# Optimization experiments

Measured on AMD Instinct MI355X. Metric: run time of the kernel, lower is better.

## Reference

```python
import jax, jax.numpy as jnp
import numpy as np

HIDDEN = 768
HEADS = 12
HEAD_DIM = HIDDEN // HEADS


def setup_inputs() -> dict:
    key = jax.random.key(0)
    ks = jax.random.split(key, 6)
    B, N = 32, 577  # N = 1 CLS + 576 patches
    x = jax.random.normal(ks[0], (B, N, HIDDEN), dtype=jnp.float32)
    seg_bias = jax.random.uniform(ks[1], (B, N - 1), dtype=jnp.float32)
    w_qkv = jax.random.normal(ks[2], (HIDDEN, 3 * HIDDEN), dtype=jnp.float32) * 0.02
    b_qkv = jnp.zeros((3 * HIDDEN,), dtype=jnp.float32)
    w_proj = jax.random.normal(ks[3], (HIDDEN, HIDDEN), dtype=jnp.float32) * 0.02
    b_proj = jnp.zeros((HIDDEN,), dtype=jnp.float32)
    seg_scale = jnp.ones((), dtype=jnp.float32)
    return {"x": x, "seg_bias": seg_bias, "w_qkv": w_qkv, "b_qkv": b_qkv,
            "w_proj": w_proj, "b_proj": b_proj, "seg_scale": seg_scale}


def reference(x, seg_bias, w_qkv, b_qkv, w_proj, b_proj, seg_scale):
    B, N, _ = x.shape
    scale = HEAD_DIM ** -0.5
    qkv = x @ w_qkv + b_qkv                       # (B, N, 3*H*D)
    qkv = qkv.reshape(B, N, 3, HEADS, HEAD_DIM)
    q = qkv[:, :, 0].transpose(0, 2, 1, 3)        # (B, H, N, D)
    k = qkv[:, :, 1].transpose(0, 2, 1, 3)
    v = qkv[:, :, 2].transpose(0, 2, 1, 3)
    attn = jnp.einsum('bhqd,bhkd->bhqk', q, k) * scale  # (B, H, N, N)
    # additive seg bias on CLS-query row, patch keys only (cols 1:)
    bias = (seg_bias * seg_scale)[:, None, None, :]     # (B,1,1,N-1)
    attn = attn.at[:, :, 0:1, 1:].add(bias)
    attn = jax.nn.softmax(attn, axis=-1)
    out = jnp.einsum('bhqk,bhkd->bhqd', attn, v)        # (B, H, N, D)
    out = out.transpose(0, 2, 1, 3).reshape(B, N, HIDDEN)
    return out @ w_proj + b_proj
```

## Files before the change

### kernel.cpp

```cpp
#include <hip/hip_runtime.h>


typedef unsigned short bf16_t;
typedef __attribute__((ext_vector_type(8))) short short8;
typedef __attribute__((ext_vector_type(4))) short short4v;
typedef __attribute__((ext_vector_type(4))) float f32x4;

#define B_    32
#define N_    577
#define BN_   18464
#define HID_  768
#define NH_   12
#define HD_   64
#define QKVC_ 2304
#define NPAD_ 640
#define PB_LD 68

__device__ __forceinline__ bf16_t f2bf(float f) {
  union { float f; unsigned u; } x; x.f = f;
  unsigned r = x.u + 0x7fffu + ((x.u >> 16) & 1u);
  return (bf16_t)(r >> 16);
}

__device__ __forceinline__ unsigned cvt_pk_bf16(float a, float b) {
  unsigned r;
  asm("v_cvt_pk_bf16_f32 %0, %1, %2" : "=v"(r) : "v"(a), "v"(b));
  return r;
}

__global__ __launch_bounds__(256) void cast_kernel(const float* __restrict__ in,
                                                   bf16_t* __restrict__ out, int n4) {
  int i = blockIdx.x * 256 + threadIdx.x;
  if (i >= n4) return;
  float4 v = ((const float4*)in)[i];
  ushort4 o;
  o.x = f2bf(v.x); o.y = f2bf(v.y); o.z = f2bf(v.z); o.w = f2bf(v.w);
  ((ushort4*)out)[i] = o;
}

__global__ __launch_bounds__(256) void transpose_cast_kernel(const float* __restrict__ in,
                                                             bf16_t* __restrict__ out,
                                                             int R, int C) {
  __shared__ float tile[32][33];
  int c0 = blockIdx.x * 32, r0 = blockIdx.y * 32;
  int tx = threadIdx.x, ty = threadIdx.y;
  #pragma unroll
  for (int i = ty; i < 32; i += 8)
    tile[i][tx] = in[(size_t)(r0 + i) * C + c0 + tx];
  __syncthreads();
  #pragma unroll
  for (int i = ty; i < 32; i += 8)
    out[(size_t)(c0 + i) * R + r0 + tx] = f2bf(tile[tx][i]);
}

template <int OUT_BF16>
__global__ __launch_bounds__(256, 3) void gemm_bf16_kernel(
    const bf16_t* __restrict__ A,
    const bf16_t* __restrict__ Bt,
    const float* __restrict__ bias,
    void* __restrict__ Cout,
    int M, int Nc) {
  __shared__ bf16_t As[128 * 64];
  __shared__ bf16_t Bs[128 * 64];

  const int tid  = threadIdx.x;
  const int lane = tid & 63, w = tid >> 6;
  const int quad = lane >> 4, l16 = lane & 15;

  const int Mb = (M + 127) >> 7;
  const int Nb = Nc >> 7;
  const int np_full = Mb >> 3;
  const int rem = Mb - np_full * 8;
  int bid = blockIdx.x;
  int m_blk, n_blk;
  int body = np_full * 8 * Nb;
  if (bid < body) {
    int p = bid / (8 * Nb), local = bid % (8 * Nb);
    m_blk = p * 8 + (local & 7);
    n_blk = local >> 3;
  } else {
    int t = bid - body;
    m_blk = np_full * 8 + t % rem;
    n_blk = t / rem;
  }
  const int m0 = m_blk * 128, n0 = n_blk * 128;
  const int wm = (w >> 1) * 64, wn = (w & 1) * 64;

  f32x4 acc[4][4];
  #pragma unroll
  for (int i = 0; i < 4; ++i)
    #pragma unroll
    for (int j = 0; j < 4; ++j)
      acc[i][j] = (f32x4){0.f, 0.f, 0.f, 0.f};

  for (int kt = 0; kt < 768; kt += 64) {
    __syncthreads();
    #pragma unroll
    for (int it = 0; it < 4; ++it) {
      int gi = it * 256 + tid;
      int row = gi >> 3, chp = gi & 7;
      int ch = chp ^ (row & 7);
      int gm = m0 + row; if (gm >= M) gm = M - 1;
      __builtin_amdgcn_global_load_lds(
          (const __attribute__((address_space(1))) unsigned int*)(A + (size_t)gm * 768 + kt + ch * 8),
          (__attribute__((address_space(3))) unsigned int*)(As + gi * 8),
          16, 0, 0);
      int gn = n0 + row;
      __builtin_amdgcn_global_load_lds(
          (const __attribute__((address_space(1))) unsigned int*)(Bt + (size_t)gn * 768 + kt + ch * 8),
          (__attribute__((address_space(3))) unsigned int*)(Bs + gi * 8),
          16, 0, 0);
    }
    __syncthreads();

    #pragma unroll
    for (int ks = 0; ks < 2; ++ks) {
      short8 af[4], bfr[4];
      #pragma unroll
      for (int i = 0; i < 4; ++i) {
        int row = wm + i * 16 + l16;
        int c = ks * 4 + quad;
        af[i] = *(const short8*)(As + row * 64 + (c ^ (row & 7)) * 8);
      }
      #pragma unroll
      for (int j = 0; j < 4; ++j) {
        int row = wn + j * 16 + l16;
        int c = ks * 4 + quad;
        bfr[j] = *(const short8*)(Bs + row * 64 + (c ^ (row & 7)) * 8);
      }
      #pragma unroll
      for (int i = 0; i < 4; ++i)
        #pragma unroll
        for (int j = 0; j < 4; ++j)
          acc[i][j] = __builtin_amdgcn_mfma_f32_16x16x32_bf16(af[i], bfr[j], acc[i][j], 0, 0, 0);
    }
  }

  #pragma unroll
  for (int i = 0; i < 4; ++i) {
    int mrow_base = m0 + wm + i * 16 + quad * 4;
    #pragma unroll
    for (int j = 0; j < 4; ++j) {
      int col = n0 + wn + j * 16 + l16;
      float bs = bias[col];
      #pragma unroll
      for (int r = 0; r < 4; ++r) {
        int row = mrow_base + r;
        if (row < M) {
          float v = acc[i][j][r] + bs;
          if (OUT_BF16)
            ((bf16_t*)Cout)[(size_t)row * Nc + col] = f2bf(v);
          else
            ((float*)Cout)[(size_t)row * Nc + col] = v;
        }
      }
    }
  }
}

__global__ __launch_bounds__(256) void vt_kernel(const bf16_t* __restrict__ qkv,
                                                 bf16_t* __restrict__ vT) {
  const int t = blockIdx.x, h = blockIdx.y, b = blockIdx.z;
  const int tid = threadIdx.x;
  __shared__ bf16_t Ls[64 * 65];
  const int kv0 = t * 64;
  const bf16_t* Vp = qkv + (size_t)b * N_ * QKVC_ + 2 * HID_ + h * HD_;

  #pragma unroll
  for (int it = 0; it < 2; ++it) {
    int idx = it * 256 + tid;
    int row = idx >> 3, ch = idx & 7;
    int krow = kv0 + row; if (krow > N_ - 1) krow = N_ - 1;
    short8 v8 = *(const short8*)(Vp + (size_t)krow * QKVC_ + ch * 8);
    #pragma unroll
    for (int j = 0; j < 8; ++j)
      Ls[(ch * 8 + j) * 65 + row] = (bf16_t)v8[j];
  }
  __syncthreads();
  bf16_t* outp = vT + ((size_t)(b * NH_ + h) * HD_) * NPAD_;
  #pragma unroll
  for (int it = 0; it < 2; ++it) {
    int idx = it * 256 + tid;
    int d = idx >> 3, kc = idx & 7;
    short8 o8;
    #pragma unroll
    for (int j = 0; j < 8; ++j) {
      int p = kc * 8 + j;
      int ky = ((p & 3) << 4) | (p >> 2);
      o8[j] = (short)Ls[d * 65 + ky];
    }
    *(short8*)(outp + (size_t)d * NPAD_ + kv0 + kc * 8) = o8;
  }
}

template <int MI>
__device__ __forceinline__ void attn_body(
    int b, int h, int qbase,
    const bf16_t* __restrict__ qkv, const bf16_t* __restrict__ vT,
    const float* __restrict__ seg_bias, const float* __restrict__ seg_scale,
    bf16_t* __restrict__ out,
    bf16_t* Ks0, bf16_t* Ks1, bf16_t* Vt0, bf16_t* Vt1, bf16_t* PbAll) {
  const int tid = threadIdx.x;
  const int w = tid >> 6, lane = tid & 63;
  const int quad = lane >> 4, l16 = lane & 15;
  const int xsw = l16 & 7;

  const bf16_t* Qbase = qkv + (size_t)b * N_ * QKVC_ + h * HD_;
  const bf16_t* Kbase = Qbase + HID_;
  const bf16_t* Vtb   = vT + ((size_t)(b * NH_ + h) * HD_) * NPAD_;

  const float ssl = seg_scale[0] * 1.44269504f;

  {
    int row = tid >> 3;
    int ch = (tid & 7) ^ (row & 7);
    __builtin_amdgcn_global_load_lds(
        (const __attribute__((address_space(1))) unsigned int*)(Kbase + (size_t)row * QKVC_ + ch * 8),
        (__attribute__((address_space(3))) unsigned int*)(Ks0 + tid * 8), 16, 0, 0);
    __builtin_amdgcn_global_load_lds(
        (const __attribute__((address_space(1))) unsigned int*)(Vtb + (size_t)row * NPAD_ + ch * 8),
        (__attribute__((address_space(3))) unsigned int*)(Vt0 + tid * 8), 16, 0, 0);
  }

  const int q0 = qbase + w * (MI * 16);
  short8 qf[MI][2];
  #pragma unroll
  for (int mi = 0; mi < MI; ++mi) {
    int qr = q0 + mi * 16 + l16;
    if (qr > N_ - 1) qr = N_ - 1;
    qf[mi][0] = *(const short8*)(Qbase + (size_t)qr * QKVC_ + quad * 8);
    qf[mi][1] = *(const short8*)(Qbase + (size_t)qr * QKVC_ + 32 + quad * 8);
  }
  const float qsc = 0.125f * 1.44269504f;
  #pragma unroll
  for (int mi = 0; mi < MI; ++mi)
    #pragma unroll
    for (int c = 0; c < 2; ++c)
      #pragma unroll
      for (int j = 0; j < 8; ++j) {
        unsigned u = ((unsigned)(unsigned short)qf[mi][c][j]) << 16;
        union { unsigned u; float f; } x; x.u = u;
        qf[mi][c][j] = (short)f2bf(x.f * qsc);
      }

  const f32x4 z4 = {0.f, 0.f, 0.f, 0.f};
  f32x4 o[MI][4];
  f32x4 ls[MI];
  #pragma unroll
  for (int mi = 0; mi < MI; ++mi) {
    ls[mi] = z4;
    #pragma unroll
    for (int j = 0; j < 4; ++j) o[mi][j] = z4;
  }

  short8 ones;
  #pragma unroll
  for (int j = 0; j < 8; ++j) ones[j] = (short)0x3F80;

  const bool bias_wave = (qbase == 0 && w == 0);
  bf16_t* pw = PbAll + w * 16 * PB_LD;

  for (int t = 0; t < 9; ++t) {
    const int cur = t & 1;

    __builtin_amdgcn_s_barrier();
    __builtin_amdgcn_sched_barrier(0);

    {
      const int kv1 = (t + 1) * 64;
      bf16_t* ksn = cur ? Ks0 : Ks1;
      bf16_t* vtn = cur ? Vt0 : Vt1;
      int row = tid >> 3;
      int ch = (tid & 7) ^ (row & 7);
      int krow = kv1 + row; if (krow > N_ - 1) krow = N_ - 1;
      __builtin_amdgcn_global_load_lds(
          (const __attribute__((address_space(1))) unsigned int*)(Kbase + (size_t)krow * QKVC_ + ch * 8),
          (__attribute__((address_space(3))) unsigned int*)(ksn + tid * 8), 16, 0, 0);
      __builtin_amdgcn_global_load_lds(
          (const __attribute__((address_space(1))) unsigned int*)(Vtb + (size_t)row * NPAD_ + kv1 + ch * 8),
          (__attribute__((address_space(3))) unsigned int*)(vtn + tid * 8), 16, 0, 0);
    }

    asm volatile("s_waitcnt vmcnt(2)" ::: "memory");
    __builtin_amdgcn_sched_barrier(0);
    __builtin_amdgcn_s_barrier();
    __builtin_amdgcn_sched_barrier(0);

    const bf16_t* ks = cur ? Ks1 : Ks0;
    const bf16_t* vt = cur ? Vt1 : Vt0;

    f32x4 s[MI][4];
    __builtin_amdgcn_s_setprio(1);
    #pragma unroll
    for (int sub = 0; sub < 4; ++sub) {
      short8 k0 = *(const short8*)(ks + (sub * 16 + l16) * 64 + (quad ^ xsw) * 8);
      short8 k1 = *(const short8*)(ks + (sub * 16 + l16) * 64 + ((4 + quad) ^ xsw) * 8);
      #pragma unroll
      for (int mi = 0; mi < MI; ++mi) {
        s[mi][sub] = __builtin_amdgcn_mfma_f32_16x16x32_bf16(qf[mi][0], k0, z4, 0, 0, 0);
        s[mi][sub] = __builtin_amdgcn_mfma_f32_16x16x32_bf16(qf[mi][1], k1, s[mi][sub], 0, 0, 0);
      }
    }
    __builtin_amdgcn_s_setprio(0);

    if (bias_wave && quad == 0) {
      const int kv0 = t * 64;
      #pragma unroll
      for (int sub = 0; sub < 4; ++sub) {
        int key = kv0 + sub * 16 + l16;
        if (key >= 1)
          s[0][sub][0] += seg_bias[b * (N_ - 1) + key - 1] * ssl;
      }
    }

    #pragma unroll
    for (int mi = 0; mi < MI; ++mi) {
      #pragma unroll
      for (int r = 0; r < 4; ++r) {
        float p0 = __builtin_amdgcn_exp2f(s[mi][0][r]);
        float p1 = __builtin_amdgcn_exp2f(s[mi][1][r]);
        float p2 = __builtin_amdgcn_exp2f(s[mi][2][r]);
        float p3 = __builtin_amdgcn_exp2f(s[mi][3][r]);
        uint2 pk;
        pk.x = cvt_pk_bf16(p0, p1);
        pk.y = cvt_pk_bf16(p2, p3);
        *(uint2*)(pw + (quad * 4 + r) * PB_LD + l16 * 4) = pk;
      }

      const bf16_t* pr = pw + l16 * PB_LD + quad * 8;
      union { short8 v; short4v hv[2]; } pa0, pa1;
      pa0.hv[0] = *(const short4v*)(pr);
      pa0.hv[1] = *(const short4v*)(pr + 4);
      pa1.hv[0] = *(const short4v*)(pr + 32);
      pa1.hv[1] = *(const short4v*)(pr + 36);
      __builtin_amdgcn_s_setprio(1);
      ls[mi] = __builtin_amdgcn_mfma_f32_16x16x32_bf16(pa0.v, ones, ls[mi], 0, 0, 0);
      ls[mi] = __builtin_amdgcn_mfma_f32_16x16x32_bf16(pa1.v, ones, ls[mi], 0, 0, 0);
      #pragma unroll
      for (int ds = 0; ds < 4; ++ds) {
        short8 vb0 = *(const short8*)(vt + (ds * 16 + l16) * 64 + (quad ^ xsw) * 8);
        short8 vb1 = *(const short8*)(vt + (ds * 16 + l16) * 64 + ((4 + quad) ^ xsw) * 8);
        o[mi][ds] = __builtin_amdgcn_mfma_f32_16x16x32_bf16(pa0.v, vb0, o[mi][ds], 0, 0, 0);
        o[mi][ds] = __builtin_amdgcn_mfma_f32_16x16x32_bf16(pa1.v, vb1, o[mi][ds], 0, 0, 0);
      }
      __builtin_amdgcn_s_setprio(0);
    }
  }

  {
    asm volatile("s_waitcnt vmcnt(0)" ::: "memory");
    __builtin_amdgcn_sched_barrier(0);
    __builtin_amdgcn_s_barrier();
    __builtin_amdgcn_sched_barrier(0);

    const bf16_t* ks = Ks1;
    const bf16_t* vt = Vt1;

    short8 k0 = *(const short8*)(ks + l16 * 64 + (quad ^ xsw) * 8);
    short8 k1 = *(const short8*)(ks + l16 * 64 + ((4 + quad) ^ xsw) * 8);
    f32x4 s9[MI];
    #pragma unroll
    for (int mi = 0; mi < MI; ++mi) {
      s9[mi] = __builtin_amdgcn_mfma_f32_16x16x32_bf16(qf[mi][0], k0, z4, 0, 0, 0);
      s9[mi] = __builtin_amdgcn_mfma_f32_16x16x32_bf16(qf[mi][1], k1, s9[mi], 0, 0, 0);
    }
    if (bias_wave && quad == 0 && l16 == 0)
      s9[0][0] += seg_bias[b * (N_ - 1) + (N_ - 2)] * ssl;

    #pragma unroll
    for (int mi = 0; mi < MI; ++mi) {
      #pragma unroll
      for (int r = 0; r < 4; ++r) {
        float p0 = (l16 == 0) ? __builtin_amdgcn_exp2f(s9[mi][r]) : 0.f;
        uint2 pk;
        pk.x = cvt_pk_bf16(p0, 0.f);
        pk.y = 0u;
        *(uint2*)(pw + (quad * 4 + r) * PB_LD + l16 * 4) = pk;
      }
      const bf16_t* pr = pw + l16 * PB_LD + quad * 8;
      union { short8 v; short4v hv[2]; } pa0;
      pa0.hv[0] = *(const short4v*)(pr);
      pa0.hv[1] = *(const short4v*)(pr + 4);
      ls[mi] = __builtin_amdgcn_mfma_f32_16x16x32_bf16(pa0.v, ones, ls[mi], 0, 0, 0);
      #pragma unroll
      for (int ds = 0; ds < 4; ++ds) {
        short8 vb0 = *(const short8*)(vt + (ds * 16 + l16) * 64 + (quad ^ xsw) * 8);
        o[mi][ds] = __builtin_amdgcn_mfma_f32_16x16x32_bf16(pa0.v, vb0, o[mi][ds], 0, 0, 0);
      }
    }
  }

  #pragma unroll
  for (int mi = 0; mi < MI; ++mi)
    #pragma unroll
    for (int r = 0; r < 4; ++r) {
      float inv = 1.0f / ls[mi][r];
      int row = q0 + mi * 16 + quad * 4 + r;
      if (row < N_) {
        size_t base = ((size_t)b * N_ + row) * HID_ + h * HD_;
        #pragma unroll
        for (int ds = 0; ds < 4; ++ds)
          out[base + ds * 16 + l16] = f2bf(o[mi][ds][r] * inv);
      }
    }
}

__global__ __launch_bounds__(512) void attn_kernel(
    const bf16_t* __restrict__ qkv,
    const bf16_t* __restrict__ vT,
    const float* __restrict__ seg_bias,
    const float* __restrict__ seg_scale,
    bf16_t* __restrict__ out) {
  __shared__ __align__(16) bf16_t Ks[2][64 * 64];
  __shared__ __align__(16) bf16_t Vt[2][64 * 64];
  __shared__ __align__(16) bf16_t Pb[8][16 * PB_LD];

  const int bid = blockIdx.x;
  if (bid < 768) {
    const int pair = bid % 384, qblk = bid / 384;
    attn_body<2>(pair / NH_, pair % NH_, qblk * 256,
                 qkv, vT, seg_bias, seg_scale, out,
                 &Ks[0][0], &Ks[1][0], &Vt[0][0], &Vt[1][0], &Pb[0][0]);
  } else {
    const int pair = bid - 768;
    attn_body<1>(pair / NH_, pair % NH_, 512,
                 qkv, vT, seg_bias, seg_scale, out,
                 &Ks[0][0], &Ks[1][0], &Vt[0][0], &Vt[1][0], &Pb[0][0]);
  }
}

extern "C" void kernel_launch(void* const* d_in, const int* in_sizes, int n_in,
                              void* d_out, int out_size, void* d_ws, size_t ws_size,
                              hipStream_t stream) {
  const float* x         = (const float*)d_in[0];
  const float* seg_bias  = (const float*)d_in[1];
  const float* w_qkv     = (const float*)d_in[2];
  const float* b_qkv     = (const float*)d_in[3];
  const float* w_proj    = (const float*)d_in[4];
  const float* b_proj    = (const float*)d_in[5];
  const float* seg_scale = (const float*)d_in[6];

  char* ws = (char*)d_ws;
  bf16_t* xb     = (bf16_t*)ws;
  bf16_t* wqkvT  = (bf16_t*)(ws + 28360704);
  bf16_t* wprojT = (bf16_t*)(ws + 31899648);
  bf16_t* qkvb   = (bf16_t*)(ws + 33079296);
  bf16_t* vT     = (bf16_t*)(ws + 118161408);
  bf16_t* attnb  = xb;

  cast_kernel<<<(BN_ * HID_ / 4) / 256, 256, 0, stream>>>(x, xb, BN_ * HID_ / 4);
  dim3 tb(32, 8);
  transpose_cast_kernel<<<dim3(QKVC_ / 32, HID_ / 32), tb, 0, stream>>>(w_qkv, wqkvT, HID_, QKVC_);
  transpose_cast_kernel<<<dim3(HID_ / 32, HID_ / 32), tb, 0, stream>>>(w_proj, wprojT, HID_, HID_);

  gemm_bf16_kernel<1><<<145 * (QKVC_ / 128), 256, 0, stream>>>(
      xb, wqkvT, b_qkv, (void*)qkvb, BN_, QKVC_);

  vt_kernel<<<dim3(10, NH_, B_), 256, 0, stream>>>(qkvb, vT);

  attn_kernel<<<1152, 512, 0, stream>>>(qkvb, vT, seg_bias, seg_scale, attnb);

  gemm_bf16_kernel<0><<<145 * (HID_ / 128), 256, 0, stream>>>(
      attnb, wprojT, b_proj, d_out, BN_, HID_);
}
```

Measured before the change: 302.3 us.

## Use 256x256 double-buffered GEMM tiles with async LDS prefetch

The bf16 GEMM kernel moves from 128x128 tiles with 256 threads to 256x256 tiles with 512 threads. Shared memory is double-buffered and the next K-slices are prefetched through global_load_lds, with explicit vmcnt waits and barriers in place of sync-load-sync. MFMA sections are wrapped in setprio. The aim is more data reuse per tile and overlap of global loads with compute, at the cost of 1 block per CU and coarse tiles that waste work on the M tail (18464 rows) and give fewer blocks for the 768-wide projection GEMM.

```diff
diff --git a/kernel.cpp b/kernel.cpp
--- a/kernel.cpp
+++ b/kernel.cpp
@@ -53,22 +53,43 @@
     out[(size_t)(c0 + i) * R + r0 + tx] = f2bf(tile[tx][i]);
 }
 
+__device__ __forceinline__ void stage256(const bf16_t* __restrict__ A,
+                                         const bf16_t* __restrict__ Bt,
+                                         int M, int m0, int n0, int kt,
+                                         bf16_t* as, bf16_t* bs, int tid) {
+  #pragma unroll
+  for (int it = 0; it < 4; ++it) {
+    int gi = it * 512 + tid;
+    int row = gi >> 3;
+    int ch = (gi & 7) ^ (row & 7);
+    int gm = m0 + row; if (gm >= M) gm = M - 1;
+    __builtin_amdgcn_global_load_lds(
+        (const __attribute__((address_space(1))) unsigned int*)(A + (size_t)gm * 768 + kt + ch * 8),
+        (__attribute__((address_space(3))) unsigned int*)(as + gi * 8), 16, 0, 0);
+    int gn = n0 + row;
+    __builtin_amdgcn_global_load_lds(
+        (const __attribute__((address_space(1))) unsigned int*)(Bt + (size_t)gn * 768 + kt + ch * 8),
+        (__attribute__((address_space(3))) unsigned int*)(bs + gi * 8), 16, 0, 0);
+  }
+}
+
 template <int OUT_BF16>
-__global__ __launch_bounds__(256, 3) void gemm_bf16_kernel(
+__global__ __launch_bounds__(512, 1) void gemm_bf16_kernel(
     const bf16_t* __restrict__ A,
     const bf16_t* __restrict__ Bt,
     const float* __restrict__ bias,
     void* __restrict__ Cout,
     int M, int Nc) {
-  __shared__ bf16_t As[128 * 64];
-  __shared__ bf16_t Bs[128 * 64];
+  __shared__ __align__(16) bf16_t As[2][256 * 64];
+  __shared__ __align__(16) bf16_t Bs[2][256 * 64];
 
   const int tid  = threadIdx.x;
   const int lane = tid & 63, w = tid >> 6;
   const int quad = lane >> 4, l16 = lane & 15;
-
-  const int Mb = (M + 127) >> 7;
-  const int Nb = Nc >> 7;
+  const int xsw = l16 & 7;
+
+  const int Mb = (M + 255) >> 8;
+  const int Nb = Nc >> 8;
   const int np_full = Mb >> 3;
   const int rem = Mb - np_full * 8;
   int bid = blockIdx.x;
@@ -79,75 +100,72 @@
     m_blk = p * 8 + (local & 7);
     n_blk = local >> 3;
   } else {
-    int t = bid - body;
-    m_blk = np_full * 8 + t % rem;
-    n_blk = t / rem;
-  }
-  const int m0 = m_blk * 128, n0 = n_blk * 128;
-  const int wm = (w >> 1) * 64, wn = (w & 1) * 64;
-
-  f32x4 acc[4][4];
-  #pragma unroll
-  for (int i = 0; i < 4; ++i)
+    int t2 = bid - body;
+    m_blk = np_full * 8 + t2 % rem;
+    n_blk = t2 / rem;
+  }
+  const int m0 = m_blk * 256, n0 = n_blk * 256;
+  const int wm = (w >> 2) * 128, wn = (w & 3) * 64;
+
+  f32x4 acc[8][4];
+  #pragma unroll
+  for (int i = 0; i < 8; ++i)
     #pragma unroll
     for (int j = 0; j < 4; ++j)
       acc[i][j] = (f32x4){0.f, 0.f, 0.f, 0.f};
 
-  for (int kt = 0; kt < 768; kt += 64) {
-    __syncthreads();
-    #pragma unroll
-    for (int it = 0; it < 4; ++it) {
-      int gi = it * 256 + tid;
-      int row = gi >> 3, chp = gi & 7;
-      int ch = chp ^ (row & 7);
-      int gm = m0 + row; if (gm >= M) gm = M - 1;
-      __builtin_amdgcn_global_load_lds(
-          (const __attribute__((address_space(1))) unsigned int*)(A + (size_t)gm * 768 + kt + ch * 8),
-          (__attribute__((address_space(3))) unsigned int*)(As + gi * 8),
-          16, 0, 0);
-      int gn = n0 + row;
-      __builtin_amdgcn_global_load_lds(
-          (const __attribute__((address_space(1))) unsigned int*)(Bt + (size_t)gn * 768 + kt + ch * 8),
-          (__attribute__((address_space(3))) unsigned int*)(Bs + gi * 8),
-          16, 0, 0);
-    }
-    __syncthreads();
+  stage256(A, Bt, M, m0, n0, 0,  &As[0][0], &Bs[0][0], tid);
+  stage256(A, Bt, M, m0, n0, 64, &As[1][0], &Bs[1][0], tid);
+
+  for (int t = 0; t < 12; ++t) {
+    bf16_t* as = &As[t & 1][0];
+    bf16_t* bs = &Bs[t & 1][0];
+
+    if (t == 11) asm volatile("s_waitcnt vmcnt(0)" ::: "memory");
+    else         asm volatile("s_waitcnt vmcnt(8)" ::: "memory");
+    __builtin_amdgcn_sched_barrier(0);
+    __builtin_amdgcn_s_barrier();
+    __builtin_amdgcn_sched_barrier(0);
 
     #pragma unroll
     for (int ks = 0; ks < 2; ++ks) {
-      short8 af[4], bfr[4];
-      #pragma unroll
-      for (int i = 0; i < 4; ++i) {
-        int row = wm + i * 16 + l16;
-        int c = ks * 4 + quad;
-        af[i] = *(const short8*)(As + row * 64 + (c ^ (row & 7)) * 8);
-      }
-      #pragma unroll
-      for (int j = 0; j < 4; ++j) {
-        int row = wn + j * 16 + l16;
-        int c = ks * 4 + quad;
-        bfr[j] = *(const short8*)(Bs + row * 64 + (c ^ (row & 7)) * 8);
-      }
-      #pragma unroll
-      for (int i = 0; i < 4; ++i)
+      const int c = (ks * 4 + quad) ^ xsw;
+      short8 af[8], bfr[4];
+      #pragma unroll
+      for (int i = 0; i < 8; ++i)
+        af[i] = *(const short8*)(as + (wm + i * 16 + l16) * 64 + c * 8);
+      #pragma unroll
+      for (int j = 0; j < 4; ++j)
+        bfr[j] = *(const short8*)(bs + (wn + j * 16 + l16) * 64 + c * 8);
+      __builtin_amdgcn_s_setprio(1);
+      #pragma unroll
+      for (int i = 0; i < 8; ++i)
         #pragma unroll
         for (int j = 0; j < 4; ++j)
           acc[i][j] = __builtin_amdgcn_mfma_f32_16x16x32_bf16(af[i], bfr[j], acc[i][j], 0, 0, 0);
-    }
-  }
-
-  #pragma unroll
-  for (int i = 0; i < 4; ++i) {
+      __builtin_amdgcn_s_setprio(0);
+    }
+
+    if (t < 10) {
+      __builtin_amdgcn_sched_barrier(0);
+      __builtin_amdgcn_s_barrier();
+      __builtin_amdgcn_sched_barrier(0);
+      stage256(A, Bt, M, m0, n0, (t + 2) * 64, as, bs, tid);
+    }
+  }
+
+  #pragma unroll
+  for (int i = 0; i < 8; ++i) {
     int mrow_base = m0 + wm + i * 16 + quad * 4;
     #pragma unroll
     for (int j = 0; j < 4; ++j) {
       int col = n0 + wn + j * 16 + l16;
-      float bs = bias[col];
+      float bs_ = bias[col];
       #pragma unroll
       for (int r = 0; r < 4; ++r) {
         int row = mrow_base + r;
         if (row < M) {
-          float v = acc[i][j][r] + bs;
+          float v = acc[i][j][r] + bs_;
           if (OUT_BF16)
             ((bf16_t*)Cout)[(size_t)row * Nc + col] = f2bf(v);
           else
@@ -453,13 +471,13 @@
   transpose_cast_kernel<<<dim3(QKVC_ / 32, HID_ / 32), tb, 0, stream>>>(w_qkv, wqkvT, HID_, QKVC_);
   transpose_cast_kernel<<<dim3(HID_ / 32, HID_ / 32), tb, 0, stream>>>(w_proj, wprojT, HID_, HID_);
 
-  gemm_bf16_kernel<1><<<145 * (QKVC_ / 128), 256, 0, stream>>>(
+  gemm_bf16_kernel<1><<<73 * (QKVC_ / 256), 512, 0, stream>>>(
       xb, wqkvT, b_qkv, (void*)qkvb, BN_, QKVC_);
 
   vt_kernel<<<dim3(10, NH_, B_), 256, 0, stream>>>(qkvb, vT);
 
   attn_kernel<<<1152, 512, 0, stream>>>(qkvb, vT, seg_bias, seg_scale, attnb);
 
-  gemm_bf16_kernel<0><<<145 * (HID_ / 128), 256, 0, stream>>>(
+  gemm_bf16_kernel<0><<<73 * (HID_ / 256), 512, 0, stream>>>(
       attnb, wprojT, b_proj, d_out, BN_, HID_);
 }
```

New measurement: 330.7 us. 9.4% more time.

## Fuse fp32-to-bf16 input cast into QKV GEMM tile loads and merge weight transposes

Applied to the files above, without the earlier changes.

Removes the standalone cast kernel for x by having the QKV GEMM load fp32 rows directly, convert them with packed bf16 instructions and store into swizzled LDS. The two weight transpose-cast launches are merged into one grid using a z dimension. This avoids a full write and reread of a bf16 copy of x plus one launch. In exchange the GEMM's A loads become synchronous register loads of twice the bytes instead of async global-to-LDS transfers.

```diff
diff --git a/kernel.cpp b/kernel.cpp
--- a/kernel.cpp
+++ b/kernel.cpp
@@ -28,19 +28,18 @@
   return r;
 }
 
-__global__ __launch_bounds__(256) void cast_kernel(const float* __restrict__ in,
-                                                   bf16_t* __restrict__ out, int n4) {
-  int i = blockIdx.x * 256 + threadIdx.x;
-  if (i >= n4) return;
-  float4 v = ((const float4*)in)[i];
-  ushort4 o;
-  o.x = f2bf(v.x); o.y = f2bf(v.y); o.z = f2bf(v.z); o.w = f2bf(v.w);
-  ((ushort4*)out)[i] = o;
-}
-
-__global__ __launch_bounds__(256) void transpose_cast_kernel(const float* __restrict__ in,
-                                                             bf16_t* __restrict__ out,
-                                                             int R, int C) {
+__global__ __launch_bounds__(256) void transpose_cast2_kernel(
+    const float* __restrict__ w_qkv, bf16_t* __restrict__ wqkvT,
+    const float* __restrict__ w_proj, bf16_t* __restrict__ wprojT) {
+  const float* in;
+  bf16_t* out;
+  int C;
+  if (blockIdx.z == 0) { in = w_qkv;  out = wqkvT;  C = QKVC_; }
+  else {
+    if (blockIdx.x >= HID_ / 32) return;
+    in = w_proj; out = wprojT; C = HID_;
+  }
+  const int R = HID_;
   __shared__ float tile[32][33];
   int c0 = blockIdx.x * 32, r0 = blockIdx.y * 32;
   int tx = threadIdx.x, ty = threadIdx.y;
@@ -53,9 +52,9 @@
     out[(size_t)(c0 + i) * R + r0 + tx] = f2bf(tile[tx][i]);
 }
 
-template <int OUT_BF16>
+template <int OUT_BF16, int A_FP32>
 __global__ __launch_bounds__(256, 3) void gemm_bf16_kernel(
-    const bf16_t* __restrict__ A,
+    const void* __restrict__ Ain,
     const bf16_t* __restrict__ Bt,
     const float* __restrict__ bias,
     void* __restrict__ Cout,
@@ -95,21 +94,51 @@
 
   for (int kt = 0; kt < 768; kt += 64) {
     __syncthreads();
-    #pragma unroll
-    for (int it = 0; it < 4; ++it) {
-      int gi = it * 256 + tid;
-      int row = gi >> 3, chp = gi & 7;
-      int ch = chp ^ (row & 7);
-      int gm = m0 + row; if (gm >= M) gm = M - 1;
-      __builtin_amdgcn_global_load_lds(
-          (const __attribute__((address_space(1))) unsigned int*)(A + (size_t)gm * 768 + kt + ch * 8),
-          (__attribute__((address_space(3))) unsigned int*)(As + gi * 8),
-          16, 0, 0);
-      int gn = n0 + row;
-      __builtin_amdgcn_global_load_lds(
-          (const __attribute__((address_space(1))) unsigned int*)(Bt + (size_t)gn * 768 + kt + ch * 8),
-          (__attribute__((address_space(3))) unsigned int*)(Bs + gi * 8),
-          16, 0, 0);
+    if (A_FP32) {
+      #pragma unroll
+      for (int it = 0; it < 4; ++it) {
+        int gi = it * 256 + tid;
+        int row = gi >> 3, chp = gi & 7;
+        int ch = chp ^ (row & 7);
+        int gn = n0 + row;
+        __builtin_amdgcn_global_load_lds(
+            (const __attribute__((address_space(1))) unsigned int*)(Bt + (size_t)gn * 768 + kt + ch * 8),
+            (__attribute__((address_space(3))) unsigned int*)(Bs + gi * 8),
+            16, 0, 0);
+      }
+      #pragma unroll
+      for (int it = 0; it < 4; ++it) {
+        int gi = it * 256 + tid;
+        int row = gi >> 3, chp = gi & 7;
+        int gm = m0 + row; if (gm >= M) gm = M - 1;
+        const float* src = (const float*)Ain + (size_t)gm * 768 + kt + chp * 8;
+        float4 v0 = *(const float4*)(src);
+        float4 v1 = *(const float4*)(src + 4);
+        uint4 pk;
+        pk.x = cvt_pk_bf16(v0.x, v0.y);
+        pk.y = cvt_pk_bf16(v0.z, v0.w);
+        pk.z = cvt_pk_bf16(v1.x, v1.y);
+        pk.w = cvt_pk_bf16(v1.z, v1.w);
+        int ch = chp ^ (row & 7);
+        *(uint4*)(As + row * 64 + ch * 8) = pk;
+      }
+    } else {
+      #pragma unroll
+      for (int it = 0; it < 4; ++it) {
+        int gi = it * 256 + tid;
+        int row = gi >> 3, chp = gi & 7;
+        int ch = chp ^ (row & 7);
+        int gm = m0 + row; if (gm >= M) gm = M - 1;
+        __builtin_amdgcn_global_load_lds(
+            (const __attribute__((address_space(1))) unsigned int*)((const bf16_t*)Ain + (size_t)gm * 768 + kt + ch * 8),
+            (__attribute__((address_space(3))) unsigned int*)(As + gi * 8),
+            16, 0, 0);
+        int gn = n0 + row;
+        __builtin_amdgcn_global_load_lds(
+            (const __attribute__((address_space(1))) unsigned int*)(Bt + (size_t)gn * 768 + kt + ch * 8),
+            (__attribute__((address_space(3))) unsigned int*)(Bs + gi * 8),
+            16, 0, 0);
+      }
     }
     __syncthreads();
 
@@ -441,25 +470,23 @@
   const float* seg_scale = (const float*)d_in[6];
 
   char* ws = (char*)d_ws;
-  bf16_t* xb     = (bf16_t*)ws;
+  bf16_t* attnb  = (bf16_t*)ws;
   bf16_t* wqkvT  = (bf16_t*)(ws + 28360704);
   bf16_t* wprojT = (bf16_t*)(ws + 31899648);
   bf16_t* qkvb   = (bf16_t*)(ws + 33079296);
   bf16_t* vT     = (bf16_t*)(ws + 118161408);
-  bf16_t* attnb  = xb;
-
-  cast_kernel<<<(BN_ * HID_ / 4) / 256, 256, 0, stream>>>(x, xb, BN_ * HID_ / 4);
+
   dim3 tb(32, 8);
-  transpose_cast_kernel<<<dim3(QKVC_ / 32, HID_ / 32), tb, 0, stream>>>(w_qkv, wqkvT, HID_, QKVC_);
-  transpose_cast_kernel<<<dim3(HID_ / 32, HID_ / 32), tb, 0, stream>>>(w_proj, wprojT, HID_, HID_);
-
-  gemm_bf16_kernel<1><<<145 * (QKVC_ / 128), 256, 0, stream>>>(
-      xb, wqkvT, b_qkv, (void*)qkvb, BN_, QKVC_);
+  transpose_cast2_kernel<<<dim3(QKVC_ / 32, HID_ / 32, 2), tb, 0, stream>>>(
+      w_qkv, wqkvT, w_proj, wprojT);
+
+  gemm_bf16_kernel<1, 1><<<145 * (QKVC_ / 128), 256, 0, stream>>>(
+      (const void*)x, wqkvT, b_qkv, (void*)qkvb, BN_, QKVC_);
 
   vt_kernel<<<dim3(10, NH_, B_), 256, 0, stream>>>(qkvb, vT);
 
   attn_kernel<<<1152, 512, 0, stream>>>(qkvb, vT, seg_bias, seg_scale, attnb);
 
-  gemm_bf16_kernel<0><<<145 * (HID_ / 128), 256, 0, stream>>>(
-      attnb, wprojT, b_proj, d_out, BN_, HID_);
-}
+  gemm_bf16_kernel<0, 0><<<145 * (HID_ / 128), 256, 0, stream>>>(
+      (const void*)attnb, wprojT, b_proj, d_out, BN_, HID_);
+}
```

Measured after the change: 341.3 us. +12.9%, slower.
